# Performance work log

Hardware: AMD Instinct MI355X
Metric: run time of the kernel (lower is better)

Reference implementation:

```python
import jax, jax.numpy as jnp
import numpy as np

B, D, NB, H = 4096, 1024, 16, 2048
LN_EPS = 1e-5


def setup_inputs() -> dict:
    key = jax.random.key(0)
    ks = jax.random.split(key, 10)
    basis_dim = D * NB
    x = jax.random.normal(ks[0], (B, D), dtype=jnp.float32)
    ln_g = jnp.ones((D,), jnp.float32)
    ln_b = jnp.zeros((D,), jnp.float32)
    centers = jnp.tile(jnp.linspace(-2.0, 2.0, NB, dtype=jnp.float32)[None, :], (D, 1))  # [D, NB]
    width = jnp.ones((D,), jnp.float32)
    fc1_w = jax.random.normal(ks[1], (H, basis_dim), jnp.float32) / np.sqrt(basis_dim)
    fc1_b = jnp.zeros((H,), jnp.float32)
    hm_w = jax.random.normal(ks[2], (1, H), jnp.float32) / np.sqrt(H)
    hm_b = jnp.zeros((1,), jnp.float32)
    hv_w = jax.random.normal(ks[3], (1, H), jnp.float32) / np.sqrt(H)
    hv_b = jnp.zeros((1,), jnp.float32)
    sh_w = jax.random.normal(ks[4], (1, D), jnp.float32) / np.sqrt(D)
    sh_b = jnp.zeros((1,), jnp.float32)
    gamma = jnp.asarray(0.3, jnp.float32)
    return {"x": x, "ln_g": ln_g, "ln_b": ln_b, "centers": centers, "width": width,
            "fc1_w": fc1_w, "fc1_b": fc1_b, "hm_w": hm_w, "hm_b": hm_b,
            "hv_w": hv_w, "hv_b": hv_b, "sh_w": sh_w, "sh_b": sh_b, "gamma": gamma}


def reference(x, ln_g, ln_b, centers, width, fc1_w, fc1_b, hm_w, hm_b, hv_w, hv_b, sh_w, sh_b, gamma):
    # LayerNorm over in_dim
    mu = jnp.mean(x, axis=-1, keepdims=True)
    var = jnp.mean(jnp.square(x - mu), axis=-1, keepdims=True)
    x_n = (x - mu) * jax.lax.rsqrt(var + LN_EPS) * ln_g + ln_b  # [B, D]
    # triangular basis: phi[b,d,k] = relu(1 - |(x_n[b,d] - c[d,k]) / w[d]|)
    w = jax.nn.softplus(width) + 1e-6                              # [D]
    phi = jax.nn.relu(1.0 - jnp.abs((x_n[:, :, None] - centers[None]) / w[None, :, None]))
    z = phi.reshape(x.shape[0], -1)                                # [B, D*NB]
    h = jax.nn.gelu(z @ fc1_w.T + fc1_b, approximate=False)        # [B, H] (dropout = eval identity)
    y_kan_mean = h @ hm_w.T + hm_b                                 # [B, 1]
    y_lin_mean = x_n @ sh_w.T + sh_b                               # [B, 1]
    mean = y_kan_mean + jax.nn.relu(gamma) * y_lin_mean
    log_var = h @ hv_w.T + hv_b
    return (mean, log_var)
```

## Files before the change

kernel.cpp:

```cpp
#include <hip/hip_runtime.h>
#include <hip/hip_bf16.h>

#define BB 4096
#define DD 1024
#define NBF 16
#define HH 2048
#define KK 16384
#define LN_EPS 1e-5f

typedef int   i32x4 __attribute__((ext_vector_type(4)));
typedef unsigned short us8 __attribute__((ext_vector_type(8)));

__device__ __forceinline__ unsigned short f2bf(float f) {
  union { float f; unsigned int u; } c; c.f = f;
  unsigned int u = c.u;
  return (unsigned short)((u + 0x7FFFu + ((u >> 16) & 1u)) >> 16);
}
__device__ __forceinline__ float bf2f(unsigned short s) {
  union { unsigned int u; float f; } c; c.u = ((unsigned int)s) << 16;
  return c.f;
}
__device__ __forceinline__ float softplusf(float x) {
  return (x > 20.f) ? x : log1pf(expf(x));
}
__device__ __forceinline__ int pack4(int q0, int q1, int q2, int q3) {
  return (q0 & 0xff) | ((q1 & 0xff) << 8) | ((q2 & 0xff) << 16) | ((q3 & 0xff) << 24);
}

__global__ void prep_kernel(const float* __restrict__ centers, const float* __restrict__ width,
                            float* __restrict__ cs) {
  const int i = blockIdx.x * 256 + threadIdx.x;
  const int d = i >> 4;
  const float w = softplusf(width[d]) + 1e-6f;
  cs[i] = centers[i] / w;
}

__global__ __launch_bounds__(256)
void zexp_kernel(const float* __restrict__ x, const float* __restrict__ g,
                 const float* __restrict__ be, const float* __restrict__ width,
                 const float* __restrict__ sh_w, const float* __restrict__ sh_b,
                 const float* __restrict__ cs,
                 unsigned char* __restrict__ zq, float* __restrict__ ylin) {
  __shared__ float red[8];
  const int b = blockIdx.x, tid = threadIdx.x;
  const float4 v = ((const float4*)(x + (size_t)b * DD))[tid];
  float s  = v.x + v.y + v.z + v.w;
  float ss = v.x*v.x + v.y*v.y + v.z*v.z + v.w*v.w;
  #pragma unroll
  for (int off = 32; off > 0; off >>= 1) {
    s  += __shfl_xor(s, off);
    ss += __shfl_xor(ss, off);
  }
  if ((tid & 63) == 0) { red[(tid>>6)*2] = s; red[(tid>>6)*2+1] = ss; }
  __syncthreads();
  const float sum   = red[0]+red[2]+red[4]+red[6];
  const float sumsq = red[1]+red[3]+red[5]+red[7];
  const float mu   = sum * (1.f/DD);
  const float var  = sumsq * (1.f/DD) - mu*mu;
  const float rstd = rsqrtf(var + LN_EPS);
  const float4 g4 = ((const float4*)g)[tid];
  const float4 b4 = ((const float4*)be)[tid];
  const float4 w4 = ((const float4*)width)[tid];
  const float4 s4 = ((const float4*)sh_w)[tid];
  const float xn0 = (v.x - mu)*rstd*g4.x + b4.x;
  const float xn1 = (v.y - mu)*rstd*g4.y + b4.y;
  const float xn2 = (v.z - mu)*rstd*g4.z + b4.z;
  const float xn3 = (v.w - mu)*rstd*g4.w + b4.w;
  float xsv[4];
  xsv[0] = xn0 / (softplusf(w4.x) + 1e-6f);
  xsv[1] = xn1 / (softplusf(w4.y) + 1e-6f);
  xsv[2] = xn2 / (softplusf(w4.z) + 1e-6f);
  xsv[3] = xn3 / (softplusf(w4.w) + 1e-6f);
  unsigned char* zr = zq + (size_t)b * KK + tid * 64;
  #pragma unroll
  for (int j = 0; j < 4; ++j) {
    const float4* c4 = (const float4*)(cs + (tid * 4 + j) * 16);
    const float xv = xsv[j];
    int q[16];
    #pragma unroll
    for (int qq = 0; qq < 4; ++qq) {
      const float4 ca = c4[qq];
      q[qq*4+0] = __float2int_rn(fmaxf(0.f, 1.f - fabsf(xv - ca.x)) * 127.f);
      q[qq*4+1] = __float2int_rn(fmaxf(0.f, 1.f - fabsf(xv - ca.y)) * 127.f);
      q[qq*4+2] = __float2int_rn(fmaxf(0.f, 1.f - fabsf(xv - ca.z)) * 127.f);
      q[qq*4+3] = __float2int_rn(fmaxf(0.f, 1.f - fabsf(xv - ca.w)) * 127.f);
    }
    int4 o;
    o.x = pack4(q[0],  q[1],  q[2],  q[3]);
    o.y = pack4(q[4],  q[5],  q[6],  q[7]);
    o.z = pack4(q[8],  q[9],  q[10], q[11]);
    o.w = pack4(q[12], q[13], q[14], q[15]);
    ((int4*)zr)[j] = o;
  }
  float yd = xn0*s4.x + xn1*s4.y + xn2*s4.z + xn3*s4.w;
  #pragma unroll
  for (int off = 32; off > 0; off >>= 1) yd += __shfl_xor(yd, off);
  __syncthreads();
  if ((tid & 63) == 0) red[tid>>6] = yd;
  __syncthreads();
  if (tid == 0) ylin[b] = red[0]+red[1]+red[2]+red[3] + sh_b[0];
}

__global__ __launch_bounds__(256)
void cvt_kernel(const float* __restrict__ w, unsigned char* __restrict__ wq,
                float* __restrict__ wscale) {
  __shared__ float red[4];
  const int j = blockIdx.x, tid = threadIdx.x;
  const float4* row4 = (const float4*)(w + (size_t)j * KK);
  float4 vv[16];
  float mx = 0.f;
  #pragma unroll
  for (int i = 0; i < 16; ++i) {
    vv[i] = row4[tid + i * 256];
    mx = fmaxf(mx, fmaxf(fmaxf(fabsf(vv[i].x), fabsf(vv[i].y)),
                         fmaxf(fabsf(vv[i].z), fabsf(vv[i].w))));
  }
  #pragma unroll
  for (int off = 32; off > 0; off >>= 1) mx = fmaxf(mx, __shfl_xor(mx, off));
  if ((tid & 63) == 0) red[tid >> 6] = mx;
  __syncthreads();
  const float smax = fmaxf(fmaxf(red[0], red[1]), fmaxf(red[2], red[3]));
  const float inv  = (smax > 0.f) ? 127.f / smax : 0.f;
  if (tid == 0) wscale[j] = smax * (1.f / 127.f);
  int* orow = (int*)(wq + (size_t)j * KK);
  #pragma unroll
  for (int i = 0; i < 16; ++i) {
    const int q0 = __float2int_rn(vv[i].x * inv);
    const int q1 = __float2int_rn(vv[i].y * inv);
    const int q2 = __float2int_rn(vv[i].z * inv);
    const int q3 = __float2int_rn(vv[i].w * inv);
    orow[tid + i * 256] = pack4(q0, q1, q2, q3);
  }
}

__global__ __launch_bounds__(256, 2)
void gemm_kernel(const unsigned char* __restrict__ zq, const unsigned char* __restrict__ wq,
                 const float* __restrict__ wscale, const float* __restrict__ fc1_b,
                 unsigned short* __restrict__ h) {
  __shared__ unsigned char As[2][128 * 128];
  __shared__ unsigned char Bs[2][128 * 128];
  const int tid  = threadIdx.x;
  const int lane = tid & 63;
  const int wv   = tid >> 6;
  const int bid = (blockIdx.x & 7) * 64 + (blockIdx.x >> 3);
  const int bm = bid & 31;
  const int bn = bid >> 5;
  const int wr = wv >> 1, wc = wv & 1;

  i32x4 acc[4][4];
  #pragma unroll
  for (int m = 0; m < 4; ++m)
    #pragma unroll
    for (int n = 0; n < 4; ++n)
      acc[m][n] = (i32x4){0, 0, 0, 0};

  const int srow   = lane >> 3;
  const int schunk = (lane & 7) ^ srow;
  const int frow = lane & 15;
  const int fkb  = lane >> 4;

  const unsigned char* zb  = zq + (size_t)(bm * 128) * KK;
  const unsigned char* wbb = wq + (size_t)(bn * 128) * KK;

  #define STAGE(buf, t) do { \
    const int k0_ = (t) * 128; \
    _Pragma("unroll") \
    for (int i_ = 0; i_ < 4; ++i_) { \
      const int r_ = i_ * 32 + wv * 8 + srow; \
      __builtin_amdgcn_global_load_lds( \
          (const __attribute__((address_space(1))) void*)(zb + (size_t)r_ * KK + k0_ + schunk * 16), \
          (__attribute__((address_space(3))) void*)(&As[buf][(i_ * 32 + wv * 8) * 128]), 16, 0, 0); \
      __builtin_amdgcn_global_load_lds( \
          (const __attribute__((address_space(1))) void*)(wbb + (size_t)r_ * KK + k0_ + schunk * 16), \
          (__attribute__((address_space(3))) void*)(&Bs[buf][(i_ * 32 + wv * 8) * 128]), 16, 0, 0); \
    } \
  } while (0)

  STAGE(0, 0);

  for (int t = 0; t < KK / 128; ++t) {
    __syncthreads();
    if (t + 1 < KK / 128) STAGE((t + 1) & 1, t + 1);
    const unsigned char* Ac = &As[t & 1][0];
    const unsigned char* Bc = &Bs[t & 1][0];
    #pragma unroll
    for (int ks = 0; ks < 2; ++ks) {
      const int kb = ks * 4 + fkb;
      i32x4 af[4], bfr[4];
      #pragma unroll
      for (int m = 0; m < 4; ++m) {
        const int Ra = wr * 64 + m * 16 + frow;
        af[m] = *reinterpret_cast<const i32x4*>(&Ac[Ra * 128 + ((kb ^ (Ra & 7)) * 16)]);
      }
      #pragma unroll
      for (int n = 0; n < 4; ++n) {
        const int Rb = wc * 64 + n * 16 + frow;
        bfr[n] = *reinterpret_cast<const i32x4*>(&Bc[Rb * 128 + ((kb ^ (Rb & 7)) * 16)]);
      }
      #pragma unroll
      for (int m = 0; m < 4; ++m)
        #pragma unroll
        for (int n = 0; n < 4; ++n)
          acc[m][n] = __builtin_amdgcn_mfma_i32_16x16x64_i8(af[m], bfr[n], acc[m][n], 0, 0, 0);
    }
  }
  #undef STAGE

  const int row0 = bm * 128 + wr * 64;
  const int col0 = bn * 128 + wc * 64;
  #pragma unroll
  for (int n = 0; n < 4; ++n) {
    const int col = col0 + n * 16 + frow;
    const float sc   = wscale[col] * (1.f / 127.f);
    const float bias = fc1_b[col];
    #pragma unroll
    for (int m = 0; m < 4; ++m) {
      #pragma unroll
      for (int r = 0; r < 4; ++r) {
        const int row = row0 + m * 16 + fkb * 4 + r;
        const float xg = (float)acc[m][n][r] * sc + bias;
        h[(size_t)row * HH + col] = f2bf(0.5f * xg * (1.f + erff(xg * 0.70710678118f)));
      }
    }
  }
}

__global__ __launch_bounds__(256)
void head_kernel(const unsigned short* __restrict__ h, const float* __restrict__ hm_w,
                 const float* __restrict__ hm_b, const float* __restrict__ hv_w,
                 const float* __restrict__ hv_b, const float* __restrict__ ylin,
                 const float* __restrict__ gamma, float* __restrict__ out) {
  __shared__ float red[8];
  const int b = blockIdx.x, tid = threadIdx.x;
  const us8 hv8 = ((const us8*)(h + (size_t)b * HH))[tid];
  const float4 m0 = ((const float4*)hm_w)[tid*2],  m1 = ((const float4*)hm_w)[tid*2+1];
  const float4 v0 = ((const float4*)hv_w)[tid*2],  v1 = ((const float4*)hv_w)[tid*2+1];
  float hf[8];
  #pragma unroll
  for (int i = 0; i < 8; ++i) hf[i] = bf2f((unsigned short)hv8[i]);
  float dm = hf[0]*m0.x + hf[1]*m0.y + hf[2]*m0.z + hf[3]*m0.w
           + hf[4]*m1.x + hf[5]*m1.y + hf[6]*m1.z + hf[7]*m1.w;
  float dv = hf[0]*v0.x + hf[1]*v0.y + hf[2]*v0.z + hf[3]*v0.w
           + hf[4]*v1.x + hf[5]*v1.y + hf[6]*v1.z + hf[7]*v1.w;
  #pragma unroll
  for (int off = 32; off > 0; off >>= 1) {
    dm += __shfl_xor(dm, off);
    dv += __shfl_xor(dv, off);
  }
  if ((tid & 63) == 0) { red[(tid>>6)*2] = dm; red[(tid>>6)*2+1] = dv; }
  __syncthreads();
  if (tid == 0) {
    const float sm = red[0]+red[2]+red[4]+red[6] + hm_b[0];
    const float sv = red[1]+red[3]+red[5]+red[7] + hv_b[0];
    out[b]      = sm + fmaxf(gamma[0], 0.f) * ylin[b];
    out[BB + b] = sv;
  }
}

extern "C" void kernel_launch(void* const* d_in, const int* in_sizes, int n_in,
                              void* d_out, int out_size, void* d_ws, size_t ws_size,
                              hipStream_t stream) {
  const float* x       = (const float*)d_in[0];
  const float* ln_g    = (const float*)d_in[1];
  const float* ln_b    = (const float*)d_in[2];
  const float* centers = (const float*)d_in[3];
  const float* width   = (const float*)d_in[4];
  const float* fc1_w   = (const float*)d_in[5];
  const float* fc1_b   = (const float*)d_in[6];
  const float* hm_w    = (const float*)d_in[7];
  const float* hm_b    = (const float*)d_in[8];
  const float* hv_w    = (const float*)d_in[9];
  const float* hv_b    = (const float*)d_in[10];
  const float* sh_w    = (const float*)d_in[11];
  const float* sh_b    = (const float*)d_in[12];
  const float* gamma   = (const float*)d_in[13];

  char* ws = (char*)d_ws;
  float* cs            = (float*)(ws);
  float* ylin          = (float*)(ws + (64 << 10));
  float* wscale        = (float*)(ws + (80 << 10));
  unsigned char* zq    = (unsigned char*)(ws + (1ull << 20));
  unsigned char* wq    = (unsigned char*)(ws + (65ull << 20));
  unsigned short* h    = (unsigned short*)(ws + (97ull << 20));
  float* out           = (float*)d_out;

  prep_kernel<<<dim3(64),   dim3(256), 0, stream>>>(centers, width, cs);
  zexp_kernel<<<dim3(4096), dim3(256), 0, stream>>>(x, ln_g, ln_b, width, sh_w, sh_b, cs, zq, ylin);
  cvt_kernel <<<dim3(2048), dim3(256), 0, stream>>>(fc1_w, wq, wscale);
  gemm_kernel<<<dim3(512),  dim3(256), 0, stream>>>(zq, wq, wscale, fc1_b, h);
  head_kernel<<<dim3(4096), dim3(256), 0, stream>>>(h, hm_w, hm_b, hv_w, hv_b, ylin, gamma, out);
}
```

Measured before the change: 223.9 us.

## Restructure int8 GEMM into 256x128 tiles with 8 waves and phased ping-pong pipeline

```diff
diff --git a/kernel.cpp b/kernel.cpp
--- a/kernel.cpp
+++ b/kernel.cpp
@@ -133,19 +133,28 @@
   }
 }
 
-__global__ __launch_bounds__(256, 2)
+__global__ __launch_bounds__(512, 1)
 void gemm_kernel(const unsigned char* __restrict__ zq, const unsigned char* __restrict__ wq,
                  const float* __restrict__ wscale, const float* __restrict__ fc1_b,
                  unsigned short* __restrict__ h) {
-  __shared__ unsigned char As[2][128 * 128];
+  __shared__ unsigned char As[2][256 * 128];
   __shared__ unsigned char Bs[2][128 * 128];
   const int tid  = threadIdx.x;
   const int lane = tid & 63;
   const int wv   = tid >> 6;
-  const int bid = (blockIdx.x & 7) * 64 + (blockIdx.x >> 3);
-  const int bm = bid & 31;
-  const int bn = bid >> 5;
-  const int wr = wv >> 1, wc = wv & 1;
+  const int wr   = wv >> 1;
+  const int wc   = wv & 1;
+  const int bid = (blockIdx.x & 7) * 32 + (blockIdx.x >> 3);
+  const int bm = bid & 15;
+  const int bn = bid >> 4;
+
+  const int srow   = lane >> 3;
+  const int schunk = (lane & 7) ^ srow;
+  const int frow = lane & 15;
+  const int fkb  = lane >> 4;
+
+  const unsigned char* zb  = zq + (size_t)(bm * 256) * KK;
+  const unsigned char* wbb = wq + (size_t)(bn * 128) * KK;
 
   i32x4 acc[4][4];
   #pragma unroll
@@ -154,59 +163,82 @@
     for (int n = 0; n < 4; ++n)
       acc[m][n] = (i32x4){0, 0, 0, 0};
 
-  const int srow   = lane >> 3;
-  const int schunk = (lane & 7) ^ srow;
-  const int frow = lane & 15;
-  const int fkb  = lane >> 4;
-
-  const unsigned char* zb  = zq + (size_t)(bm * 128) * KK;
-  const unsigned char* wbb = wq + (size_t)(bn * 128) * KK;
-
-  #define STAGE(buf, t) do { \
-    const int k0_ = (t) * 128; \
-    _Pragma("unroll") \
-    for (int i_ = 0; i_ < 4; ++i_) { \
-      const int r_ = i_ * 32 + wv * 8 + srow; \
-      __builtin_amdgcn_global_load_lds( \
-          (const __attribute__((address_space(1))) void*)(zb + (size_t)r_ * KK + k0_ + schunk * 16), \
-          (__attribute__((address_space(3))) void*)(&As[buf][(i_ * 32 + wv * 8) * 128]), 16, 0, 0); \
-      __builtin_amdgcn_global_load_lds( \
-          (const __attribute__((address_space(1))) void*)(wbb + (size_t)r_ * KK + k0_ + schunk * 16), \
-          (__attribute__((address_space(3))) void*)(&Bs[buf][(i_ * 32 + wv * 8) * 128]), 16, 0, 0); \
-    } \
+  #define STAGE_A(buf, u, j) __builtin_amdgcn_global_load_lds( \
+      (const __attribute__((address_space(1))) void*)(zb + (size_t)((j)*64 + wv*8 + srow) * KK + (size_t)(u)*128 + schunk*16), \
+      (__attribute__((address_space(3))) void*)(&As[buf][((j)*64 + wv*8) * 128]), 16, 0, 0)
+  #define STAGE_B(buf, u, hh) __builtin_amdgcn_global_load_lds( \
+      (const __attribute__((address_space(1))) void*)(wbb + (size_t)((hh)*64 + wv*8 + srow) * KK + (size_t)(u)*128 + schunk*16), \
+      (__attribute__((address_space(3))) void*)(&Bs[buf][((hh)*64 + wv*8) * 128]), 16, 0, 0)
+
+  #define RD_A2(CB, dst, mbase) do { \
+    _Pragma("unroll") for (int mm = 0; mm < 2; ++mm) { \
+      const int Ra = wr*64 + ((mbase)+mm)*16 + frow; \
+      _Pragma("unroll") for (int ks = 0; ks < 2; ++ks) { \
+        const int kb = ks*4 + fkb; \
+        dst[mm][ks] = *reinterpret_cast<const i32x4*>(&As[CB][Ra*128 + ((kb ^ (Ra&7))*16)]); \
+      } } } while (0)
+  #define RD_B2(CB, dst, nbase) do { \
+    _Pragma("unroll") for (int nn = 0; nn < 2; ++nn) { \
+      const int Rb = wc*64 + ((nbase)+nn)*16 + frow; \
+      _Pragma("unroll") for (int ks = 0; ks < 2; ++ks) { \
+        const int kb = ks*4 + fkb; \
+        dst[nn][ks] = *reinterpret_cast<const i32x4*>(&Bs[CB][Rb*128 + ((kb ^ (Rb&7))*16)]); \
+      } } } while (0)
+
+  #define BAR()  asm volatile("s_barrier" ::: "memory")
+  #define LGK0() asm volatile("s_waitcnt lgkmcnt(0)" ::: "memory")
+  #define VM2()  asm volatile("s_waitcnt vmcnt(2)" ::: "memory")
+
+  #define MF8(AF, BF, MO, NO) do { \
+    _Pragma("unroll") for (int mm = 0; mm < 2; ++mm) \
+      _Pragma("unroll") for (int nn = 0; nn < 2; ++nn) \
+        _Pragma("unroll") for (int ks = 0; ks < 2; ++ks) \
+          acc[(MO)+mm][(NO)+nn] = __builtin_amdgcn_mfma_i32_16x16x64_i8(AF[mm][ks], BF[nn][ks], acc[(MO)+mm][(NO)+nn], 0, 0, 0); \
   } while (0)
 
-  STAGE(0, 0);
-
-  for (int t = 0; t < KK / 128; ++t) {
-    __syncthreads();
-    if (t + 1 < KK / 128) STAGE((t + 1) & 1, t + 1);
-    const unsigned char* Ac = &As[t & 1][0];
-    const unsigned char* Bc = &Bs[t & 1][0];
-    #pragma unroll
-    for (int ks = 0; ks < 2; ++ks) {
-      const int kb = ks * 4 + fkb;
-      i32x4 af[4], bfr[4];
-      #pragma unroll
-      for (int m = 0; m < 4; ++m) {
-        const int Ra = wr * 64 + m * 16 + frow;
-        af[m] = *reinterpret_cast<const i32x4*>(&Ac[Ra * 128 + ((kb ^ (Ra & 7)) * 16)]);
-      }
-      #pragma unroll
-      for (int n = 0; n < 4; ++n) {
-        const int Rb = wc * 64 + n * 16 + frow;
-        bfr[n] = *reinterpret_cast<const i32x4*>(&Bc[Rb * 128 + ((kb ^ (Rb & 7)) * 16)]);
-      }
-      #pragma unroll
-      for (int m = 0; m < 4; ++m)
-        #pragma unroll
-        for (int n = 0; n < 4; ++n)
-          acc[m][n] = __builtin_amdgcn_mfma_i32_16x16x64_i8(af[m], bfr[n], acc[m][n], 0, 0, 0);
-    }
-  }
-  #undef STAGE
-
-  const int row0 = bm * 128 + wr * 64;
+  #define PH_GROUP(CB, AB, uA, BBf, uB) do { \
+    i32x4 afA[2][2], afB[2][2], bf0[2][2], bf1[2][2]; \
+     \
+    RD_A2(CB, afA, 0); RD_B2(CB, bf0, 0); \
+    STAGE_A(AB, uA, 0); STAGE_A(AB, uA, 1); \
+    BAR(); LGK0(); __builtin_amdgcn_s_setprio(1); \
+    MF8(afA, bf0, 0, 0); \
+    __builtin_amdgcn_s_setprio(0); BAR(); \
+     \
+    RD_B2(CB, bf1, 2); \
+    STAGE_A(AB, uA, 2); STAGE_A(AB, uA, 3); \
+    BAR(); LGK0(); __builtin_amdgcn_s_setprio(1); \
+    MF8(afA, bf1, 0, 2); \
+    __builtin_amdgcn_s_setprio(0); BAR(); \
+     \
+    RD_A2(CB, afB, 2); \
+    STAGE_B(BBf, uB, 0); \
+    BAR(); LGK0(); __builtin_amdgcn_s_setprio(1); \
+    MF8(afB, bf1, 2, 2); \
+    __builtin_amdgcn_s_setprio(0); BAR(); \
+     \
+    STAGE_B(BBf, uB, 1); \
+    BAR(); LGK0(); __builtin_amdgcn_s_setprio(1); \
+    MF8(afB, bf0, 2, 0); \
+    __builtin_amdgcn_s_setprio(0); \
+    VM2(); BAR(); \
+  } while (0)
+
+  STAGE_B(0, 0, 0); STAGE_B(0, 0, 1);
+  STAGE_A(0, 0, 0); STAGE_A(0, 0, 1); STAGE_A(0, 0, 2); STAGE_A(0, 0, 3);
+  STAGE_B(1, 1, 0); STAGE_B(1, 1, 1);
+  VM2(); BAR();
+
+  for (int i = 0; i < 64; ++i) {
+    const int ub = 2*i + 1;
+    const int uc = (2*i + 2 < 128) ? 2*i + 2 : 127;
+    const int ud = (2*i + 3 < 128) ? 2*i + 3 : 127;
+    PH_GROUP(0, 1, ub, 0, uc);
+    PH_GROUP(1, 0, uc, 1, ud);
+  }
+  asm volatile("s_waitcnt vmcnt(0)" ::: "memory");
+
+  const int row0 = bm * 256 + wr * 64;
   const int col0 = bn * 128 + wc * 64;
   #pragma unroll
   for (int n = 0; n < 4; ++n) {
@@ -223,6 +255,15 @@
       }
     }
   }
+  #undef STAGE_A
+  #undef STAGE_B
+  #undef RD_A2
+  #undef RD_B2
+  #undef BAR
+  #undef LGK0
+  #undef VM2
+  #undef MF8
+  #undef PH_GROUP
 }
 
 __global__ __launch_bounds__(256)
@@ -287,6 +328,6 @@
   prep_kernel<<<dim3(64),   dim3(256), 0, stream>>>(centers, width, cs);
   zexp_kernel<<<dim3(4096), dim3(256), 0, stream>>>(x, ln_g, ln_b, width, sh_w, sh_b, cs, zq, ylin);
   cvt_kernel <<<dim3(2048), dim3(256), 0, stream>>>(fc1_w, wq, wscale);
-  gemm_kernel<<<dim3(512),  dim3(256), 0, stream>>>(zq, wq, wscale, fc1_b, h);
+  gemm_kernel<<<dim3(256),  dim3(512), 0, stream>>>(zq, wq, wscale, fc1_b, h);
   head_kernel<<<dim3(4096), dim3(256), 0, stream>>>(h, hm_w, hm_b, hv_w, hv_b, ylin, gamma, out);
 }
```

Result: slower. 230.2 us (+2.8%).

## Load B fragments directly from global into registers, halving LDS staging

Applied to the files above, without the earlier changes.

```diff
diff --git a/kernel.cpp b/kernel.cpp
--- a/kernel.cpp
+++ b/kernel.cpp
@@ -6,6 +6,7 @@
 #define NBF 16
 #define HH 2048
 #define KK 16384
+#define NT 128
 #define LN_EPS 1e-5f
 
 typedef int   i32x4 __attribute__((ext_vector_type(4)));
@@ -138,7 +139,6 @@
                  const float* __restrict__ wscale, const float* __restrict__ fc1_b,
                  unsigned short* __restrict__ h) {
   __shared__ unsigned char As[2][128 * 128];
-  __shared__ unsigned char Bs[2][128 * 128];
   const int tid  = threadIdx.x;
   const int lane = tid & 63;
   const int wv   = tid >> 6;
@@ -162,49 +162,68 @@
   const unsigned char* zb  = zq + (size_t)(bm * 128) * KK;
   const unsigned char* wbb = wq + (size_t)(bn * 128) * KK;
 
-  #define STAGE(buf, t) do { \
-    const int k0_ = (t) * 128; \
+  #define STAGE_A(buf, u) do { \
+    const int k0_ = (u) * 128; \
     _Pragma("unroll") \
     for (int i_ = 0; i_ < 4; ++i_) { \
       const int r_ = i_ * 32 + wv * 8 + srow; \
       __builtin_amdgcn_global_load_lds( \
           (const __attribute__((address_space(1))) void*)(zb + (size_t)r_ * KK + k0_ + schunk * 16), \
           (__attribute__((address_space(3))) void*)(&As[buf][(i_ * 32 + wv * 8) * 128]), 16, 0, 0); \
-      __builtin_amdgcn_global_load_lds( \
-          (const __attribute__((address_space(1))) void*)(wbb + (size_t)r_ * KK + k0_ + schunk * 16), \
-          (__attribute__((address_space(3))) void*)(&Bs[buf][(i_ * 32 + wv * 8) * 128]), 16, 0, 0); \
     } \
   } while (0)
 
-  STAGE(0, 0);
-
-  for (int t = 0; t < KK / 128; ++t) {
+  #define LOADB(dst, u) do { \
+    _Pragma("unroll") \
+    for (int n_ = 0; n_ < 4; ++n_) { \
+      const int Rb_ = wc * 64 + n_ * 16 + frow; \
+      _Pragma("unroll") \
+      for (int ks_ = 0; ks_ < 2; ++ks_) { \
+        const int kb_ = ks_ * 4 + fkb; \
+        dst[n_][ks_] = *reinterpret_cast<const i32x4*>( \
+            &wbb[(size_t)Rb_ * KK + (size_t)(u) * 128 + kb_ * 16]); \
+      } \
+    } \
+  } while (0)
+
+  #define COMPUTE(buf, bset) do { \
+    _Pragma("unroll") \
+    for (int ks_ = 0; ks_ < 2; ++ks_) { \
+      const int kb_ = ks_ * 4 + fkb; \
+      i32x4 af_[4]; \
+      _Pragma("unroll") \
+      for (int m_ = 0; m_ < 4; ++m_) { \
+        const int Ra_ = wr * 64 + m_ * 16 + frow; \
+        af_[m_] = *reinterpret_cast<const i32x4*>(&As[buf][Ra_ * 128 + ((kb_ ^ (Ra_ & 7)) * 16)]); \
+      } \
+      _Pragma("unroll") \
+      for (int m_ = 0; m_ < 4; ++m_) \
+        _Pragma("unroll") \
+        for (int n_ = 0; n_ < 4; ++n_) \
+          acc[m_][n_] = __builtin_amdgcn_mfma_i32_16x16x64_i8(af_[m_], bset[n_][ks_], acc[m_][n_], 0, 0, 0); \
+    } \
+  } while (0)
+
+  i32x4 bA[4][2], bB[4][2];
+
+  STAGE_A(0, 0);
+  LOADB(bA, 0);
+
+  for (int t = 0; t < NT; t += 2) {
     __syncthreads();
-    if (t + 1 < KK / 128) STAGE((t + 1) & 1, t + 1);
-    const unsigned char* Ac = &As[t & 1][0];
-    const unsigned char* Bc = &Bs[t & 1][0];
-    #pragma unroll
-    for (int ks = 0; ks < 2; ++ks) {
-      const int kb = ks * 4 + fkb;
-      i32x4 af[4], bfr[4];
-      #pragma unroll
-      for (int m = 0; m < 4; ++m) {
-        const int Ra = wr * 64 + m * 16 + frow;
-        af[m] = *reinterpret_cast<const i32x4*>(&Ac[Ra * 128 + ((kb ^ (Ra & 7)) * 16)]);
-      }
-      #pragma unroll
-      for (int n = 0; n < 4; ++n) {
-        const int Rb = wc * 64 + n * 16 + frow;
-        bfr[n] = *reinterpret_cast<const i32x4*>(&Bc[Rb * 128 + ((kb ^ (Rb & 7)) * 16)]);
-      }
-      #pragma unroll
-      for (int m = 0; m < 4; ++m)
-        #pragma unroll
-        for (int n = 0; n < 4; ++n)
-          acc[m][n] = __builtin_amdgcn_mfma_i32_16x16x64_i8(af[m], bfr[n], acc[m][n], 0, 0, 0);
+    STAGE_A(1, t + 1);
+    LOADB(bB, t + 1);
+    COMPUTE(0, bA);
+    __syncthreads();
+    if (t + 2 < NT) {
+      STAGE_A(0, t + 2);
+      LOADB(bA, t + 2);
     }
-  }
-  #undef STAGE
+    COMPUTE(1, bB);
+  }
+  #undef STAGE_A
+  #undef LOADB
+  #undef COMPUTE
 
   const int row0 = bm * 128 + wr * 64;
   const int col0 = bn * 128 + wc * 64;
```

Result: slower. 357.0 us (+59.5%).

## Enlarge GEMM tile to 256x128 with intra-block split-K across two wave groups

Applied to the files above, without the earlier changes.

```diff
diff --git a/kernel.cpp b/kernel.cpp
--- a/kernel.cpp
+++ b/kernel.cpp
@@ -6,6 +6,7 @@
 #define NBF 16
 #define HH 2048
 #define KK 16384
+#define NT 128
 #define LN_EPS 1e-5f
 
 typedef int   i32x4 __attribute__((ext_vector_type(4)));
@@ -133,96 +134,142 @@
   }
 }
 
-__global__ __launch_bounds__(256, 2)
+__global__ __launch_bounds__(512, 1)
 void gemm_kernel(const unsigned char* __restrict__ zq, const unsigned char* __restrict__ wq,
                  const float* __restrict__ wscale, const float* __restrict__ fc1_b,
                  unsigned short* __restrict__ h) {
-  __shared__ unsigned char As[2][128 * 128];
-  __shared__ unsigned char Bs[2][128 * 128];
+  __shared__ __align__(16) unsigned char lds[98304];
+  #define A_OFF(buf) ((buf) * 32768)
+  #define B_OFF(buf) (65536 + (buf) * 16384)
+
   const int tid  = threadIdx.x;
   const int lane = tid & 63;
   const int wv   = tid >> 6;
-  const int bid = (blockIdx.x & 7) * 64 + (blockIdx.x >> 3);
-  const int bm = bid & 31;
-  const int bn = bid >> 5;
-  const int wr = wv >> 1, wc = wv & 1;
-
-  i32x4 acc[4][4];
-  #pragma unroll
-  for (int m = 0; m < 4; ++m)
-    #pragma unroll
-    for (int n = 0; n < 4; ++n)
-      acc[m][n] = (i32x4){0, 0, 0, 0};
+  const int kg   = wv >> 2;
+  const int wr   = (wv >> 1) & 1;
+  const int wc   = wv & 1;
+  const int bid = (blockIdx.x & 7) * 32 + (blockIdx.x >> 3);
+  const int bm = bid & 15;
+  const int bn = bid >> 4;
 
   const int srow   = lane >> 3;
   const int schunk = (lane & 7) ^ srow;
   const int frow = lane & 15;
   const int fkb  = lane >> 4;
 
-  const unsigned char* zb  = zq + (size_t)(bm * 128) * KK;
+  const unsigned char* zb  = zq + (size_t)(bm * 256) * KK;
   const unsigned char* wbb = wq + (size_t)(bn * 128) * KK;
+
+  i32x4 acc[8][4];
+  #pragma unroll
+  for (int m = 0; m < 8; ++m)
+    #pragma unroll
+    for (int n = 0; n < 4; ++n)
+      acc[m][n] = (i32x4){0, 0, 0, 0};
 
   #define STAGE(buf, t) do { \
     const int k0_ = (t) * 128; \
     _Pragma("unroll") \
-    for (int i_ = 0; i_ < 4; ++i_) { \
-      const int r_ = i_ * 32 + wv * 8 + srow; \
+    for (int j_ = 0; j_ < 4; ++j_) { \
+      const int r_ = j_ * 64 + wv * 8 + srow; \
       __builtin_amdgcn_global_load_lds( \
           (const __attribute__((address_space(1))) void*)(zb + (size_t)r_ * KK + k0_ + schunk * 16), \
-          (__attribute__((address_space(3))) void*)(&As[buf][(i_ * 32 + wv * 8) * 128]), 16, 0, 0); \
+          (__attribute__((address_space(3))) void*)(&lds[A_OFF(buf) + (j_ * 64 + wv * 8) * 128]), 16, 0, 0); \
+    } \
+    _Pragma("unroll") \
+    for (int j_ = 0; j_ < 2; ++j_) { \
+      const int r_ = j_ * 64 + wv * 8 + srow; \
       __builtin_amdgcn_global_load_lds( \
           (const __attribute__((address_space(1))) void*)(wbb + (size_t)r_ * KK + k0_ + schunk * 16), \
-          (__attribute__((address_space(3))) void*)(&Bs[buf][(i_ * 32 + wv * 8) * 128]), 16, 0, 0); \
+          (__attribute__((address_space(3))) void*)(&lds[B_OFF(buf) + (j_ * 64 + wv * 8) * 128]), 16, 0, 0); \
     } \
   } while (0)
 
+  #define COMPUTE(buf) do { \
+    i32x4 bfr_[4][2]; \
+    _Pragma("unroll") \
+    for (int n_ = 0; n_ < 4; ++n_) { \
+      const int Rb_ = wc * 64 + n_ * 16 + frow; \
+      _Pragma("unroll") \
+      for (int ks_ = 0; ks_ < 2; ++ks_) { \
+        const int kb_ = ks_ * 4 + fkb; \
+        bfr_[n_][ks_] = *reinterpret_cast<const i32x4*>( \
+            &lds[B_OFF(buf) + Rb_ * 128 + ((kb_ ^ (Rb_ & 7)) * 16)]); \
+      } \
+    } \
+    _Pragma("unroll") \
+    for (int m_ = 0; m_ < 8; ++m_) { \
+      const int Ra_ = wr * 128 + m_ * 16 + frow; \
+      i32x4 a0_ = *reinterpret_cast<const i32x4*>( \
+          &lds[A_OFF(buf) + Ra_ * 128 + (((fkb) ^ (Ra_ & 7)) * 16)]); \
+      i32x4 a1_ = *reinterpret_cast<const i32x4*>( \
+          &lds[A_OFF(buf) + Ra_ * 128 + (((4 + fkb) ^ (Ra_ & 7)) * 16)]); \
+      _Pragma("unroll") \
+      for (int n_ = 0; n_ < 4; ++n_) { \
+        acc[m_][n_] = __builtin_amdgcn_mfma_i32_16x16x64_i8(a0_, bfr_[n_][0], acc[m_][n_], 0, 0, 0); \
+        acc[m_][n_] = __builtin_amdgcn_mfma_i32_16x16x64_i8(a1_, bfr_[n_][1], acc[m_][n_], 0, 0, 0); \
+      } \
+    } \
+  } while (0)
+
   STAGE(0, 0);
 
-  for (int t = 0; t < KK / 128; ++t) {
+  for (int t2 = 0; t2 < 64; ++t2) {
+    const int t = 2 * t2;
     __syncthreads();
-    if (t + 1 < KK / 128) STAGE((t + 1) & 1, t + 1);
-    const unsigned char* Ac = &As[t & 1][0];
-    const unsigned char* Bc = &Bs[t & 1][0];
-    #pragma unroll
-    for (int ks = 0; ks < 2; ++ks) {
-      const int kb = ks * 4 + fkb;
-      i32x4 af[4], bfr[4];
+    STAGE(1, t + 1);
+    if (kg == 0) COMPUTE(0);
+    __syncthreads();
+    if (t + 2 < NT) STAGE(0, t + 2);
+    if (kg == 1) COMPUTE(1);
+  }
+  #undef STAGE
+  #undef COMPUTE
+
+  __syncthreads();
+  int* ldsi = (int*)lds;
+  const int p = wr * 2 + wc;
+  #pragma unroll
+  for (int c = 0; c < 2; ++c) {
+    if (kg == 1) {
       #pragma unroll
-      for (int m = 0; m < 4; ++m) {
-        const int Ra = wr * 64 + m * 16 + frow;
-        af[m] = *reinterpret_cast<const i32x4*>(&Ac[Ra * 128 + ((kb ^ (Ra & 7)) * 16)]);
-      }
-      #pragma unroll
-      for (int n = 0; n < 4; ++n) {
-        const int Rb = wc * 64 + n * 16 + frow;
-        bfr[n] = *reinterpret_cast<const i32x4*>(&Bc[Rb * 128 + ((kb ^ (Rb & 7)) * 16)]);
-      }
-      #pragma unroll
-      for (int m = 0; m < 4; ++m)
+      for (int mm = 0; mm < 4; ++mm)
         #pragma unroll
         for (int n = 0; n < 4; ++n)
-          acc[m][n] = __builtin_amdgcn_mfma_i32_16x16x64_i8(af[m], bfr[n], acc[m][n], 0, 0, 0);
+          *reinterpret_cast<i32x4*>(&ldsi[p * 4096 + (mm * 4 + n) * 256 + lane * 4]) = acc[c * 4 + mm][n];
     }
-  }
-  #undef STAGE
-
-  const int row0 = bm * 128 + wr * 64;
-  const int col0 = bn * 128 + wc * 64;
-  #pragma unroll
-  for (int n = 0; n < 4; ++n) {
-    const int col = col0 + n * 16 + frow;
-    const float sc   = wscale[col] * (1.f / 127.f);
-    const float bias = fc1_b[col];
+    __syncthreads();
+    if (kg == 0) {
+      #pragma unroll
+      for (int mm = 0; mm < 4; ++mm)
+        #pragma unroll
+        for (int n = 0; n < 4; ++n)
+          acc[c * 4 + mm][n] += *reinterpret_cast<const i32x4*>(&ldsi[p * 4096 + (mm * 4 + n) * 256 + lane * 4]);
+    }
+    __syncthreads();
+  }
+
+  if (kg == 0) {
+    const int row0 = bm * 256 + wr * 128;
+    const int col0 = bn * 128 + wc * 64;
     #pragma unroll
-    for (int m = 0; m < 4; ++m) {
+    for (int n = 0; n < 4; ++n) {
+      const int col = col0 + n * 16 + frow;
+      const float sc   = wscale[col] * (1.f / 127.f);
+      const float bias = fc1_b[col];
       #pragma unroll
-      for (int r = 0; r < 4; ++r) {
-        const int row = row0 + m * 16 + fkb * 4 + r;
-        const float xg = (float)acc[m][n][r] * sc + bias;
-        h[(size_t)row * HH + col] = f2bf(0.5f * xg * (1.f + erff(xg * 0.70710678118f)));
+      for (int m = 0; m < 8; ++m) {
+        #pragma unroll
+        for (int r = 0; r < 4; ++r) {
+          const int row = row0 + m * 16 + fkb * 4 + r;
+          const float xg = (float)acc[m][n][r] * sc + bias;
+          h[(size_t)row * HH + col] = f2bf(0.5f * xg * (1.f + erff(xg * 0.70710678118f)));
+        }
       }
     }
   }
+  #undef A_OFF
+  #undef B_OFF
 }
 
 __global__ __launch_bounds__(256)
@@ -287,6 +334,6 @@
   prep_kernel<<<dim3(64),   dim3(256), 0, stream>>>(centers, width, cs);
   zexp_kernel<<<dim3(4096), dim3(256), 0, stream>>>(x, ln_g, ln_b, width, sh_w, sh_b, cs, zq, ylin);
   cvt_kernel <<<dim3(2048), dim3(256), 0, stream>>>(fc1_w, wq, wscale);
-  gemm_kernel<<<dim3(512),  dim3(256), 0, stream>>>(zq, wq, wscale, fc1_b, h);
+  gemm_kernel<<<dim3(256),  dim3(512), 0, stream>>>(zq, wq, wscale, fc1_b, h);
   head_kernel<<<dim3(4096), dim3(256), 0, stream>>>(h, hm_w, hm_b, hv_w, hv_b, ylin, gamma, out);
 }
```

Result: slower. 232.9 us (+4.0%).
